# Kernel tuning notes

Measured on AMD Instinct MI355X. Metric: run time of the kernel, lower is better.

The kernel has to match this reference:

```python
import jax, jax.numpy as jnp
import numpy as np


def setup_inputs() -> dict:
    key = jax.random.key(0)
    B, S, H, O, L, NH = 16, 1024, 1024, 256, 4, 8
    ks = jax.random.split(key, 10)
    s = 0.02
    return {
        "x": jax.random.normal(ks[0], (B, S, H), dtype=jnp.float32),
        "Wf": jax.random.normal(ks[1], (L, H, H), dtype=jnp.float32) * s,
        "bf": jnp.zeros((L, H), dtype=jnp.float32),
        "Wi": jax.random.normal(ks[2], (L, H, H), dtype=jnp.float32) * s,
        "bi": jnp.zeros((L, H), dtype=jnp.float32),
        "Wh": jax.random.normal(ks[3], (L, H, H), dtype=jnp.float32) * s,
        "bh": jnp.zeros((L, H), dtype=jnp.float32),
        "in_proj_w": jax.random.normal(ks[4], (3 * H, H), dtype=jnp.float32) * s,
        "in_proj_b": jnp.zeros((3 * H,), dtype=jnp.float32),
        "out_w": jax.random.normal(ks[5], (H, H), dtype=jnp.float32) * s,
        "out_b": jnp.zeros((H,), dtype=jnp.float32),
        "fc_w": jax.random.normal(ks[6], (O, H), dtype=jnp.float32) * s,
        "fc_b": jnp.zeros((O,), dtype=jnp.float32),
    }


def _min_lstm_layer(x, Wf, bf, Wi, bi, Wh, bh):
    # x: [B, S, D] -> [B, S, H]. minLSTM: h_t = f'_t * h_{t-1} + i'_t * h~_t
    f = jax.nn.sigmoid(jnp.einsum("bsd,hd->bsh", x, Wf) + bf)
    i = jax.nn.sigmoid(jnp.einsum("bsd,hd->bsh", x, Wi) + bi)
    h_tilde = jnp.einsum("bsd,hd->bsh", x, Wh) + bh
    denom = f + i
    fp = f / denom                      # decay coefficient per step
    add = (i / denom) * h_tilde         # input contribution per step
    # sequential scan over time (linear gated recurrence)
    def step(h, inp):
        fp_t, add_t = inp               # each [B, H]
        h = fp_t * h + add_t
        return h, h
    B, S, H = fp.shape
    h0 = jnp.zeros((B, H), dtype=x.dtype)
    _, hs = jax.lax.scan(step, h0, (fp.transpose(1, 0, 2), add.transpose(1, 0, 2)))
    return hs.transpose(1, 0, 2)        # [B, S, H]


def _mhsa(x, in_proj_w, in_proj_b, out_w, out_b, num_heads=8):
    B, S, H = x.shape
    dh = H // num_heads
    qkv = jnp.einsum("bsh,oh->bso", x, in_proj_w) + in_proj_b  # [B,S,3H]
    q, k, v = jnp.split(qkv, 3, axis=-1)
    def heads(t):
        return t.reshape(B, S, num_heads, dh).transpose(0, 2, 1, 3)  # [B,nh,S,dh]
    q, k, v = heads(q), heads(k), heads(v)
    scores = jnp.einsum("bnqd,bnkd->bnqk", q, k) / jnp.sqrt(jnp.float32(dh)).astype(x.dtype)
    attn = jax.nn.softmax(scores, axis=-1)
    o = jnp.einsum("bnqk,bnkd->bnqd", attn, v)
    o = o.transpose(0, 2, 1, 3).reshape(B, S, H)
    return jnp.einsum("bsh,oh->bso", o, out_w) + out_b


def reference(x, Wf, bf, Wi, bi, Wh, bh, in_proj_w, in_proj_b, out_w, out_b, fc_w, fc_b):
    out = x
    L = Wf.shape[0]
    for l in range(L):
        out = _min_lstm_layer(out, Wf[l], bf[l], Wi[l], bi[l], Wh[l], bh[l])
    attn_out = _mhsa(out, in_proj_w, in_proj_b, out_w, out_b, num_heads=8)
    out = attn_out + out                 # dropout is identity at eval
    last = out[:, -1, :]                 # [B, H]
    return jnp.einsum("bh,oh->bo", last, fc_w) + fc_b
```

## Files before the change

kernel.cpp:

```cpp
#include <hip/hip_runtime.h>
#include <hip/hip_bf16.h>
#include <math.h>

#define Bq   16
#define Sq   1024
#define Hq   1024
#define Oq   256
#define Lq   4
#define NHq  8
#define DHq  128
#define Mq   (Bq*Sq)
#define HHq  (Hq*Hq)
#define NCc  32
#define CTc  32

typedef __bf16 bf16x8 __attribute__((ext_vector_type(8)));
typedef float  f32x4  __attribute__((ext_vector_type(4)));

__device__ __forceinline__ float bf2f(unsigned int u) {
    union { unsigned int i; float f; } x; x.i = u << 16; return x.f;
}
__device__ __forceinline__ unsigned short f2bf(float f) {
    union { float f; unsigned int i; } x; x.f = f;
    unsigned int r = x.i + 0x7fffu + ((x.i >> 16) & 1u);
    return (unsigned short)(r >> 16);
}
__device__ __forceinline__ float sigm(float x) { return 1.f / (1.f + __expf(-x)); }

__device__ __forceinline__ void gl2lds16(const unsigned short* g, unsigned short* l) {
    __builtin_amdgcn_global_load_lds((const __attribute__((address_space(1))) void*)g,
                                     (__attribute__((address_space(3))) void*)l, 16, 0, 0);
}

__global__ void cvt_kernel(const float* __restrict__ src, unsigned short* __restrict__ dst, int n) {
    int i = blockIdx.x * 256 + threadIdx.x;
    if (i < n) dst[i] = f2bf(src[i]);
}

__global__ void cvtW_kernel(const float* __restrict__ Wf, const float* __restrict__ Wi,
                            const float* __restrict__ Wh, unsigned short* __restrict__ Wcat) {
    int i = blockIdx.x * 256 + threadIdx.x;
    int l = (i >> 20) / 3;
    int r = i - l * 3 * HHq;
    int g = r >> 20; int j = r & (HHq - 1);
    const float* s = (g == 0) ? Wf : (g == 1) ? Wi : Wh;
    Wcat[i] = f2bf(s[(size_t)l * HHq + j]);
}

__global__ void bias3_kernel(const float* __restrict__ bf_, const float* __restrict__ bi_,
                             const float* __restrict__ bh_, float* __restrict__ out) {
    int i = blockIdx.x * 256 + threadIdx.x;
    int l = i / (3*Hq); int r = i % (3*Hq); int g = r >> 10; int j = r & (Hq-1);
    const float* s = (g == 0) ? bf_ : (g == 1) ? bi_ : bh_;
    out[i] = s[l*Hq + j];
}

__global__ __launch_bounds__(512, 1)
void gemm_gate_kernel(const unsigned short* __restrict__ A, const unsigned short* __restrict__ Wl,
                      const float* __restrict__ bias3, unsigned int* __restrict__ FA,
                      float* __restrict__ Ps, float* __restrict__ Asum)
{
    const int K = Hq;
    __shared__ unsigned short lds[4 * 20480];
    const int tid  = threadIdx.x;

    const int lid = blockIdx.x;
    const int xcd = lid & 7;
    const int s   = lid >> 3;
    const int bm  = xcd * 8 + (s >> 3);
    const int cb  = s & 7;

    const int wid  = tid >> 6, lane = tid & 63;
    const int wm   = (wid >> 2) * 128;
    const int wn   = (wid & 3) * 32;
    const int l15  = lane & 15, quad = lane >> 4;

    const unsigned short* Ag = A + (size_t)(bm*256) * K;

    const int lr   = lane >> 2;
    const int gc   = (lane & 3) ^ ((lane >> 3) & 3);
    int offA[2], ldsA[2];
    #pragma unroll
    for (int q = 0; q < 2; ++q) {
        int ra = wid*32 + q*16 + lr;
        offA[q] = ra * K + gc*8;
        ldsA[q] = (wid*32 + q*16) * 32;
    }
    int offW[3], ldsW[3];
    #pragma unroll
    for (int q = 0; q < 3; ++q) {
        int rw = wid*48 + q*16 + lr;
        int g  = rw >> 7;
        int nr = rw & 127;
        offW[q] = g * HHq + (cb*128 + nr) * K + gc*8;
        ldsW[q] = 8192 + (wid*48 + q*16) * 32;
    }

    const int crd = quad ^ ((l15 >> 1) & 3);

    f32x4 acc[3][8][2] = {};

    auto STAGE = [&](int kt, int slot) {
        const int kof = kt << 5;
        unsigned short* Sb = &lds[slot * 20480];
        #pragma unroll
        for (int q = 0; q < 2; ++q) gl2lds16(Ag + offA[q] + kof, Sb + ldsA[q]);
        #pragma unroll
        for (int q = 0; q < 3; ++q) gl2lds16(Wl + offW[q] + kof, Sb + ldsW[q]);
    };

    auto COMPUTE = [&](int slot) {
        const unsigned short* Sa = &lds[slot * 20480];
        const unsigned short* Sw = Sa + 8192;
        bf16x8 af[8];
        #pragma unroll
        for (int t = 0; t < 8; ++t)
            af[t] = *(const bf16x8*)&Sa[(wm + t*16 + l15)*32 + crd*8];
        __builtin_amdgcn_s_setprio(1);
        #pragma unroll
        for (int g = 0; g < 3; ++g) {
            bf16x8 wf[2];
            #pragma unroll
            for (int t = 0; t < 2; ++t)
                wf[t] = *(const bf16x8*)&Sw[(g*128 + wn + t*16 + l15)*32 + crd*8];
            #pragma unroll
            for (int tm = 0; tm < 8; ++tm)
                #pragma unroll
                for (int tn = 0; tn < 2; ++tn)
                    acc[g][tm][tn] = __builtin_amdgcn_mfma_f32_16x16x32_bf16(af[tm], wf[tn], acc[g][tm][tn], 0, 0, 0);
        }
        __builtin_amdgcn_s_setprio(0);
    };

    const int niter = K >> 5;

    STAGE(0, 0);
    STAGE(1, 1);

    for (int t = 0; t < niter - 2; ++t) {
        STAGE(t + 2, (t + 2) & 3);
        asm volatile("s_waitcnt vmcnt(10) lgkmcnt(0)" ::: "memory");
        __builtin_amdgcn_s_barrier();
        asm volatile("" ::: "memory");
        COMPUTE(t & 3);
    }
    asm volatile("s_waitcnt vmcnt(5) lgkmcnt(0)" ::: "memory");
    __builtin_amdgcn_s_barrier();
    asm volatile("" ::: "memory");
    COMPUTE((niter - 2) & 3);
    asm volatile("s_waitcnt vmcnt(0) lgkmcnt(0)" ::: "memory");
    __builtin_amdgcn_s_barrier();
    asm volatile("" ::: "memory");
    COMPUTE((niter - 1) & 3);

    const int colc0 = cb*128 + wn + l15;
    const int colc1 = colc0 + 16;
    float bf0 = bias3[colc0],      bf1 = bias3[colc1];
    float bi0 = bias3[Hq+colc0],   bi1 = bias3[Hq+colc1];
    float bh0 = bias3[2*Hq+colc0], bh1 = bias3[2*Hq+colc1];

    const int b_ = bm >> 2;
    const int chunkBase = (bm & 3) * 8 + (wm >> 5);

    #pragma unroll
    for (int cc = 0; cc < 4; ++cc) {
        float sP[2][2] = {{1.f,1.f},{1.f,1.f}};
        float sA[2][2] = {{0.f,0.f},{0.f,0.f}};
        #pragma unroll
        for (int sg = 0; sg < 2; ++sg) {
            int tm   = cc*2 + sg;
            int row0 = bm*256 + wm + tm*16 + quad*4;
            #pragma unroll
            for (int r = 0; r < 4; ++r) {
                #pragma unroll
                for (int tn = 0; tn < 2; ++tn) {
                    float bfv_ = tn ? bf1 : bf0;
                    float biv_ = tn ? bi1 : bi0;
                    float bhv_ = tn ? bh1 : bh0;
                    int   col  = tn ? colc1 : colc0;
                    float f  = sigm(acc[0][tm][tn][r] + bfv_);
                    float i  = sigm(acc[1][tm][tn][r] + biv_);
                    float ht = acc[2][tm][tn][r] + bhv_;
                    float rd = 1.f / (f + i);
                    unsigned short ufp = f2bf(f * rd);
                    unsigned short uad = f2bf(i * rd * ht);
                    FA[(size_t)(row0 + r) * Hq + col] =
                        (unsigned int)ufp | ((unsigned int)uad << 16);
                    float fpq = bf2f((unsigned int)ufp);
                    float adq = bf2f((unsigned int)uad);
                    sA[tn][sg] = fpq * sA[tn][sg] + adq;
                    sP[tn][sg] *= fpq;
                }
            }
        }
        int chunk  = chunkBase + cc;
        int oibase = (b_*NCc + chunk) * Hq;
        #pragma unroll
        for (int tn = 0; tn < 2; ++tn) {
            float P0 = sP[tn][0], A0 = sA[tn][0];
            float P1 = sP[tn][1], A1 = sA[tn][1];
            float pp, aa;
            pp = __shfl_up(P0, 16); aa = __shfl_up(A0, 16);
            if (quad >= 1) { A0 = P0*aa + A0; P0 = P0*pp; }
            pp = __shfl_up(P0, 32); aa = __shfl_up(A0, 32);
            if (quad >= 2) { A0 = P0*aa + A0; P0 = P0*pp; }
            pp = __shfl_up(P1, 16); aa = __shfl_up(A1, 16);
            if (quad >= 1) { A1 = P1*aa + A1; P1 = P1*pp; }
            pp = __shfl_up(P1, 32); aa = __shfl_up(A1, 32);
            if (quad >= 2) { A1 = P1*aa + A1; P1 = P1*pp; }
            float P0t = __shfl(P0, 48 + l15); float A0t = __shfl(A0, 48 + l15);
            float P1t = __shfl(P1, 48 + l15); float A1t = __shfl(A1, 48 + l15);
            if (quad == 0) {
                int col = tn ? colc1 : colc0;
                Ps[oibase + col]   = P1t * P0t;
                Asum[oibase + col] = P1t * A0t + A1t;
            }
        }
    }
}

__global__ __launch_bounds__(256, 2)
void gemm_bt_kernel(const unsigned short* __restrict__ A, const unsigned short* __restrict__ W,
                    const float* __restrict__ bias, unsigned short* __restrict__ C,
                    int N, int K, int nbn)
{
    __shared__ unsigned short lds[4 * 8192];
    const int tid  = threadIdx.x;

    const int lid = blockIdx.x;
    const int xcd = lid & 7;
    const int s   = lid >> 3;
    const int bm  = xcd * 16 + s / nbn;
    const int bn  = s % nbn;

    const int wid  = tid >> 6, lane = tid & 63;
    const int wm   = (wid >> 1) * 64, wn = (wid & 1) * 64;
    const int l15  = lane & 15, quad = lane >> 4;

    const unsigned short* Ag = A + (size_t)(bm*128) * K;
    const unsigned short* Wg = W + (size_t)(bn*128) * K;

    const int r0   = wid*32 + (lane >> 2);
    const int cst  = (lane & 3) ^ ((r0 >> 1) & 3);
    const int g0   = r0 * K + cst*8;
    const int g1   = (r0 + 16) * K + cst*8;
    const int lofs0 = wid*1024;
    const int lofs1 = wid*1024 + 512;

    const int crd = quad ^ ((l15 >> 1) & 3);

    f32x4 acc[4][4] = {};

    auto STAGE = [&](int kt, int slot) {
        const int kof = kt << 5;
        unsigned short* Sb = &lds[slot * 8192];
        gl2lds16(Ag + g0 + kof, Sb + lofs0);
        gl2lds16(Ag + g1 + kof, Sb + lofs1);
        gl2lds16(Wg + g0 + kof, Sb + 4096 + lofs0);
        gl2lds16(Wg + g1 + kof, Sb + 4096 + lofs1);
    };

    auto COMPUTE = [&](int slot) {
        const unsigned short* Sa = &lds[slot * 8192];
        const unsigned short* Sw = Sa + 4096;
        bf16x8 af[4], wf[4];
        #pragma unroll
        for (int t = 0; t < 4; ++t) {
            af[t] = *(const bf16x8*)&Sa[(wm + t*16 + l15)*32 + crd*8];
            wf[t] = *(const bf16x8*)&Sw[(wn + t*16 + l15)*32 + crd*8];
        }
        __builtin_amdgcn_s_setprio(1);
        #pragma unroll
        for (int tm = 0; tm < 4; ++tm)
            #pragma unroll
            for (int tn = 0; tn < 4; ++tn)
                acc[tm][tn] = __builtin_amdgcn_mfma_f32_16x16x32_bf16(af[tm], wf[tn], acc[tm][tn], 0, 0, 0);
        __builtin_amdgcn_s_setprio(0);
    };

    const int niter = K >> 5;

    STAGE(0, 0);
    STAGE(1, 1);

    for (int it = 0; it < niter - 2; ++it) {
        STAGE(it + 2, (it + 2) & 3);
        asm volatile("s_waitcnt vmcnt(8) lgkmcnt(0)" ::: "memory");
        __builtin_amdgcn_s_barrier();
        asm volatile("" ::: "memory");
        COMPUTE(it & 3);
    }
    asm volatile("s_waitcnt vmcnt(4) lgkmcnt(0)" ::: "memory");
    __builtin_amdgcn_s_barrier();
    asm volatile("" ::: "memory");
    COMPUTE((niter - 2) & 3);
    asm volatile("s_waitcnt vmcnt(0) lgkmcnt(0)" ::: "memory");
    __builtin_amdgcn_s_barrier();
    asm volatile("" ::: "memory");
    COMPUTE((niter - 1) & 3);

    #pragma unroll
    for (int tm = 0; tm < 4; ++tm) {
        int row0 = bm*128 + wm + tm*16 + quad*4;
        #pragma unroll
        for (int tn = 0; tn < 4; ++tn) {
            int col = bn*128 + wn + tn*16 + l15;
            float bv = bias[col];
            #pragma unroll
            for (int r = 0; r < 4; ++r)
                C[(size_t)(row0 + r) * N + col] = f2bf(acc[tm][tn][r] + bv);
        }
    }
}

__global__ void scan_base_kernel(const float* __restrict__ Ps, const float* __restrict__ Asum,
                                 float* __restrict__ Hb) {
    int t = blockIdx.x * 256 + threadIdx.x;
    int b = t >> 10, j = t & 1023;
    float h = 0.f;
    for (int c = 0; c < NCc; ++c) {
        int idx = (b*NCc + c)*Hq + j;
        Hb[idx] = h;
        h = Ps[idx] * h + Asum[idx];
    }
}

__global__ __launch_bounds__(256)
void scan_out_kernel(const unsigned int* __restrict__ FA,
                     const float* __restrict__ Hb, unsigned short* __restrict__ Ho) {
    int bid = blockIdx.x;
    int tid = threadIdx.x;
    int b = bid >> 6; int r = bid & 63; int chunk = r >> 1; int jb = r & 1;
    int j = jb*512 + tid*2;
    size_t base = ((size_t)(b*Sq + chunk*CTc)) * Hq + j;
    int oi = (b*NCc + chunk)*Hq + j;
    float h0 = Hb[oi], h1 = Hb[oi+1];
    for (int s = 0; s < CTc; ++s) {
        size_t ro = base + (size_t)s * Hq;
        uint2 v = *(const uint2*)(FA + ro);
        h0 = bf2f(v.x & 0xffffu) * h0 + bf2f(v.x >> 16);
        h1 = bf2f(v.y & 0xffffu) * h1 + bf2f(v.y >> 16);
        unsigned int packed = (unsigned int)f2bf(h0) | ((unsigned int)f2bf(h1) << 16);
        *(unsigned int*)(Ho + ro) = packed;
    }
}

__global__ void xlast_kernel(const unsigned short* __restrict__ act, float* __restrict__ xl) {
    int i = blockIdx.x * 256 + threadIdx.x;
    int b = i >> 10, j = i & 1023;
    xl[i] = bf2f((unsigned int)act[((size_t)(b*Sq + Sq-1)) * Hq + j]);
}

__global__ __launch_bounds__(256)
void gemv_kernel(const float* __restrict__ W, const float* __restrict__ xv,
                 const float* __restrict__ bias, const float* __restrict__ resid,
                 float* __restrict__ out, int N) {
    int b = blockIdx.x;
    int w = threadIdx.x >> 6, lane = threadIdx.x & 63;
    int n = blockIdx.y*4 + w;
    __shared__ float xs[Hq];
    *(float4*)&xs[threadIdx.x*4] = *(const float4*)&xv[(size_t)b*Hq + threadIdx.x*4];
    __syncthreads();
    const float4* wr = (const float4*)(W + (size_t)n * Hq);
    float a = 0.f;
    #pragma unroll
    for (int c = 0; c < 4; ++c) {
        float4 wv = wr[c*64 + lane];
        float4 x4 = *(const float4*)&xs[c*256 + lane*4];
        a += wv.x*x4.x + wv.y*x4.y + wv.z*x4.z + wv.w*x4.w;
    }
    #pragma unroll
    for (int st = 32; st > 0; st >>= 1) a += __shfl_xor(a, st, 64);
    if (lane == 0) out[(size_t)b*N + n] = a + bias[n] + (resid ? resid[(size_t)b*Hq + n] : 0.f);
}

__global__ __launch_bounds__(1024)
void attn_kernel(const unsigned short* __restrict__ KV,
                 const float* __restrict__ q, float* __restrict__ o) {
    int b = blockIdx.x >> 3, nh = blockIdx.x & 7;
    int tid = threadIdx.x;
    __shared__ float qs[DHq];
    __shared__ float p[Sq];
    __shared__ float redw[16];
    __shared__ float red2[16*DHq];
    if (tid < DHq) qs[tid] = q[b*Hq + nh*DHq + tid] * 0.08838834764831845f;
    __syncthreads();

    const int g = tid >> 4, l = tid & 15;
    const unsigned short* Kb = KV + (size_t)b*Sq*2048 + nh*DHq;
    float lmax = -1e30f;
    #pragma unroll 4
    for (int it = 0; it < 16; ++it) {
        int s = it*64 + g;
        union { uint4 v; unsigned short u[8]; } kk;
        kk.v = *(const uint4*)(Kb + (size_t)s*2048 + l*8);
        float a = 0.f;
        #pragma unroll
        for (int j = 0; j < 8; ++j) a += bf2f((unsigned int)kk.u[j]) * qs[l*8 + j];
        a += __shfl_xor(a, 1, 16);
        a += __shfl_xor(a, 2, 16);
        a += __shfl_xor(a, 4, 16);
        a += __shfl_xor(a, 8, 16);
        if (l == 0) p[s] = a;
        lmax = fmaxf(lmax, a);
    }
    #pragma unroll
    for (int st = 32; st > 0; st >>= 1) lmax = fmaxf(lmax, __shfl_xor(lmax, st, 64));
    if ((tid & 63) == 0) redw[tid >> 6] = lmax;
    __syncthreads();
    float mx = redw[0];
    #pragma unroll
    for (int i = 1; i < 16; ++i) mx = fmaxf(mx, redw[i]);

    float e = __expf(p[tid] - mx);
    float ls = e;
    #pragma unroll
    for (int st = 32; st > 0; st >>= 1) ls += __shfl_xor(ls, st, 64);
    __syncthreads();
    p[tid] = e;
    if ((tid & 63) == 0) redw[tid >> 6] = ls;
    __syncthreads();
    float ssum = 0.f;
    #pragma unroll
    for (int i = 0; i < 16; ++i) ssum += redw[i];
    float inv = 1.f / ssum;

    int d2 = (tid & 63) * 2, sb = tid >> 6;
    const unsigned short* Vb = KV + (size_t)b*Sq*2048 + 1024 + nh*DHq + d2;
    float a0 = 0.f, a1 = 0.f;
    for (int s = sb*64; s < sb*64 + 64; ++s) {
        unsigned int vv = *(const unsigned int*)(Vb + (size_t)s*2048);
        float pw = p[s];
        a0 += pw * bf2f(vv & 0xffffu);
        a1 += pw * bf2f(vv >> 16);
    }
    red2[sb*DHq + d2] = a0;
    red2[sb*DHq + d2 + 1] = a1;
    __syncthreads();
    if (tid < DHq) {
        float a = 0.f;
        #pragma unroll
        for (int i = 0; i < 16; ++i) a += red2[i*DHq + tid];
        o[b*Hq + nh*DHq + tid] = a * inv;
    }
}

extern "C" void kernel_launch(void* const* d_in, const int* in_sizes, int n_in,
                              void* d_out, int out_size, void* d_ws, size_t ws_size,
                              hipStream_t stream) {
    const float* x        = (const float*)d_in[0];
    const float* Wf       = (const float*)d_in[1];
    const float* bfv      = (const float*)d_in[2];
    const float* Wi       = (const float*)d_in[3];
    const float* biv      = (const float*)d_in[4];
    const float* Wh       = (const float*)d_in[5];
    const float* bhv      = (const float*)d_in[6];
    const float* in_proj_w= (const float*)d_in[7];
    const float* in_proj_b= (const float*)d_in[8];
    const float* out_w    = (const float*)d_in[9];
    const float* out_b    = (const float*)d_in[10];
    const float* fc_w     = (const float*)d_in[11];
    const float* fc_b     = (const float*)d_in[12];
    float* outp = (float*)d_out;

    char* p = (char*)d_ws;
    auto alloc = [&](size_t bytes) -> void* {
        void* r = (void*)p; p += (bytes + 255) & ~(size_t)255; return r;
    };
    unsigned short* Wcat = (unsigned short*)alloc((size_t)Lq*3*HHq*2);
    unsigned short* Wkv  = (unsigned short*)alloc((size_t)2048*Hq*2);
    float*          Bias3= (float*)alloc((size_t)Lq*3*Hq*4);
    unsigned short* actA = (unsigned short*)alloc((size_t)Mq*Hq*2);
    unsigned short* actB = (unsigned short*)alloc((size_t)Mq*Hq*2);
    unsigned int*   FAg  = (unsigned int*)alloc((size_t)Mq*Hq*4);
    float* Ps   = (float*)alloc((size_t)Bq*NCc*Hq*4);
    float* Asum = (float*)alloc((size_t)Bq*NCc*Hq*4);
    float* Hb   = (float*)alloc((size_t)Bq*NCc*Hq*4);
    unsigned short* KV = (unsigned short*)FAg;
    float* xl   = (float*)alloc((size_t)Bq*Hq*4);
    float* qbuf = (float*)alloc((size_t)Bq*Hq*4);
    float* obuf = (float*)alloc((size_t)Bq*Hq*4);
    float* rbuf = (float*)alloc((size_t)Bq*Hq*4);

    cvt_kernel<<<Mq*Hq/256, 256, 0, stream>>>(x, actA, Mq*Hq);
    cvtW_kernel<<<Lq*3*HHq/256, 256, 0, stream>>>(Wf, Wi, Wh, Wcat);
    cvt_kernel<<<2048*Hq/256, 256, 0, stream>>>(in_proj_w + (size_t)Hq*Hq, Wkv, 2048*Hq);
    bias3_kernel<<<(Lq*3*Hq)/256, 256, 0, stream>>>(bfv, biv, bhv, Bias3);

    unsigned short* cur = actA;
    unsigned short* nxt = actB;
    for (int l = 0; l < Lq; ++l) {
        gemm_gate_kernel<<<(Mq/256)*(Hq/128), 512, 0, stream>>>(
            cur, Wcat + (size_t)l*3*HHq, Bias3 + l*3*Hq, FAg, Ps, Asum);
        scan_base_kernel<<<Bq*Hq/256, 256, 0, stream>>>(Ps, Asum, Hb);
        scan_out_kernel<<<Bq*NCc*2, 256, 0, stream>>>(FAg, Hb, nxt);
        unsigned short* t = cur; cur = nxt; nxt = t;
    }

    gemm_bt_kernel<<<(Mq/128)*(2048/128), 256, 0, stream>>>(
        cur, Wkv, in_proj_b + Hq, KV, 2048, Hq, 2048/128);
    xlast_kernel<<<Bq*Hq/256, 256, 0, stream>>>(cur, xl);
    gemv_kernel<<<dim3(Bq, Hq/4), 256, 0, stream>>>(in_proj_w, xl, in_proj_b, nullptr, qbuf, Hq);
    attn_kernel<<<Bq*NHq, 1024, 0, stream>>>(KV, qbuf, obuf);
    gemv_kernel<<<dim3(Bq, Hq/4), 256, 0, stream>>>(out_w, obuf, out_b, xl, rbuf, Hq);
    gemv_kernel<<<dim3(Bq, Oq/4), 256, 0, stream>>>(fc_w, rbuf, fc_b, nullptr, outp, Oq);
}
```

Baseline: 815.4 us.

## Enlarge KV GEMM tile to 256x256 and fold scan base into scan output

The KV projection GEMM moves from 128x128 tiles with 4 waves to 256x256 tiles with 8 waves per block, doubling LDS staging and per-wave accumulators to raise operand reuse. The separate scan_base kernel is removed. Each scan_out block now recomputes its carry-in by serially combining the preceding chunk summaries, which saves one launch and the Hb round-trip but adds redundant work in later chunks. The larger GEMM tile raises register and LDS pressure and reduces occupancy to one block per CU.

Result: no change. 831.2 us (+1.9%).

```diff
diff --git a/kernel.cpp b/kernel.cpp
--- a/kernel.cpp
+++ b/kernel.cpp
@@ -219,59 +219,71 @@
     }
 }
 
-__global__ __launch_bounds__(256, 2)
+__global__ __launch_bounds__(512, 1)
 void gemm_bt_kernel(const unsigned short* __restrict__ A, const unsigned short* __restrict__ W,
                     const float* __restrict__ bias, unsigned short* __restrict__ C,
                     int N, int K, int nbn)
 {
-    __shared__ unsigned short lds[4 * 8192];
+    __shared__ unsigned short lds[4 * 16384];
     const int tid  = threadIdx.x;
 
     const int lid = blockIdx.x;
     const int xcd = lid & 7;
     const int s   = lid >> 3;
-    const int bm  = xcd * 16 + s / nbn;
+    const int bm  = xcd * 8 + s / nbn;
     const int bn  = s % nbn;
 
     const int wid  = tid >> 6, lane = tid & 63;
-    const int wm   = (wid >> 1) * 64, wn = (wid & 1) * 64;
+    const int wm   = (wid >> 2) * 128;
+    const int wn   = (wid & 3) * 64;
     const int l15  = lane & 15, quad = lane >> 4;
 
-    const unsigned short* Ag = A + (size_t)(bm*128) * K;
-    const unsigned short* Wg = W + (size_t)(bn*128) * K;
-
-    const int r0   = wid*32 + (lane >> 2);
-    const int cst  = (lane & 3) ^ ((r0 >> 1) & 3);
-    const int g0   = r0 * K + cst*8;
-    const int g1   = (r0 + 16) * K + cst*8;
-    const int lofs0 = wid*1024;
-    const int lofs1 = wid*1024 + 512;
+    const unsigned short* Ag = A + (size_t)(bm*256) * K;
+    const unsigned short* Wg = W + (size_t)(bn*256) * K;
+
+    const int lr   = lane >> 2;
+    const int gc   = (lane & 3) ^ ((lane >> 3) & 3);
+    int offA[2], ldsA[2];
+    #pragma unroll
+    for (int q = 0; q < 2; ++q) {
+        int ra = wid*32 + q*16 + lr;
+        offA[q] = ra * K + gc*8;
+        ldsA[q] = (wid*32 + q*16) * 32;
+    }
+    int offW[2], ldsW[2];
+    #pragma unroll
+    for (int q = 0; q < 2; ++q) {
+        int rw = wid*32 + q*16 + lr;
+        offW[q] = rw * K + gc*8;
+        ldsW[q] = 8192 + (wid*32 + q*16) * 32;
+    }
 
     const int crd = quad ^ ((l15 >> 1) & 3);
 
-    f32x4 acc[4][4] = {};
+    f32x4 acc[8][4] = {};
 
     auto STAGE = [&](int kt, int slot) {
         const int kof = kt << 5;
-        unsigned short* Sb = &lds[slot * 8192];
-        gl2lds16(Ag + g0 + kof, Sb + lofs0);
-        gl2lds16(Ag + g1 + kof, Sb + lofs1);
-        gl2lds16(Wg + g0 + kof, Sb + 4096 + lofs0);
-        gl2lds16(Wg + g1 + kof, Sb + 4096 + lofs1);
+        unsigned short* Sb = &lds[slot * 16384];
+        #pragma unroll
+        for (int q = 0; q < 2; ++q) gl2lds16(Ag + offA[q] + kof, Sb + ldsA[q]);
+        #pragma unroll
+        for (int q = 0; q < 2; ++q) gl2lds16(Wg + offW[q] + kof, Sb + ldsW[q]);
     };
 
     auto COMPUTE = [&](int slot) {
-        const unsigned short* Sa = &lds[slot * 8192];
-        const unsigned short* Sw = Sa + 4096;
-        bf16x8 af[4], wf[4];
-        #pragma unroll
-        for (int t = 0; t < 4; ++t) {
+        const unsigned short* Sa = &lds[slot * 16384];
+        const unsigned short* Sw = Sa + 8192;
+        bf16x8 af[8], wf[4];
+        #pragma unroll
+        for (int t = 0; t < 8; ++t)
             af[t] = *(const bf16x8*)&Sa[(wm + t*16 + l15)*32 + crd*8];
+        #pragma unroll
+        for (int t = 0; t < 4; ++t)
             wf[t] = *(const bf16x8*)&Sw[(wn + t*16 + l15)*32 + crd*8];
-        }
         __builtin_amdgcn_s_setprio(1);
         #pragma unroll
-        for (int tm = 0; tm < 4; ++tm)
+        for (int tm = 0; tm < 8; ++tm)
             #pragma unroll
             for (int tn = 0; tn < 4; ++tn)
                 acc[tm][tn] = __builtin_amdgcn_mfma_f32_16x16x32_bf16(af[tm], wf[tn], acc[tm][tn], 0, 0, 0);
@@ -300,11 +312,11 @@
     COMPUTE((niter - 1) & 3);
 
     #pragma unroll
-    for (int tm = 0; tm < 4; ++tm) {
-        int row0 = bm*128 + wm + tm*16 + quad*4;
+    for (int tm = 0; tm < 8; ++tm) {
+        int row0 = bm*256 + wm + tm*16 + quad*4;
         #pragma unroll
         for (int tn = 0; tn < 4; ++tn) {
-            int col = bn*128 + wn + tn*16 + l15;
+            int col = bn*256 + wn + tn*16 + l15;
             float bv = bias[col];
             #pragma unroll
             for (int r = 0; r < 4; ++r)
@@ -313,28 +325,25 @@
     }
 }
 
-__global__ void scan_base_kernel(const float* __restrict__ Ps, const float* __restrict__ Asum,
-                                 float* __restrict__ Hb) {
-    int t = blockIdx.x * 256 + threadIdx.x;
-    int b = t >> 10, j = t & 1023;
-    float h = 0.f;
-    for (int c = 0; c < NCc; ++c) {
-        int idx = (b*NCc + c)*Hq + j;
-        Hb[idx] = h;
-        h = Ps[idx] * h + Asum[idx];
-    }
-}
-
 __global__ __launch_bounds__(256)
 void scan_out_kernel(const unsigned int* __restrict__ FA,
-                     const float* __restrict__ Hb, unsigned short* __restrict__ Ho) {
+                     const float* __restrict__ Ps, const float* __restrict__ Asum,
+                     unsigned short* __restrict__ Ho) {
     int bid = blockIdx.x;
     int tid = threadIdx.x;
     int b = bid >> 6; int r = bid & 63; int chunk = r >> 1; int jb = r & 1;
     int j = jb*512 + tid*2;
     size_t base = ((size_t)(b*Sq + chunk*CTc)) * Hq + j;
-    int oi = (b*NCc + chunk)*Hq + j;
-    float h0 = Hb[oi], h1 = Hb[oi+1];
+
+    float h0 = 0.f, h1 = 0.f;
+    for (int c = 0; c < chunk; ++c) {
+        int idx = (b*NCc + c)*Hq + j;
+        float2 P = *(const float2*)&Ps[idx];
+        float2 Aa = *(const float2*)&Asum[idx];
+        h0 = P.x * h0 + Aa.x;
+        h1 = P.y * h1 + Aa.y;
+    }
+
     for (int s = 0; s < CTc; ++s) {
         size_t ro = base + (size_t)s * Hq;
         uint2 v = *(const uint2*)(FA + ro);
@@ -475,7 +484,6 @@
     unsigned int*   FAg  = (unsigned int*)alloc((size_t)Mq*Hq*4);
     float* Ps   = (float*)alloc((size_t)Bq*NCc*Hq*4);
     float* Asum = (float*)alloc((size_t)Bq*NCc*Hq*4);
-    float* Hb   = (float*)alloc((size_t)Bq*NCc*Hq*4);
     unsigned short* KV = (unsigned short*)FAg;
     float* xl   = (float*)alloc((size_t)Bq*Hq*4);
     float* qbuf = (float*)alloc((size_t)Bq*Hq*4);
@@ -492,13 +500,12 @@
     for (int l = 0; l < Lq; ++l) {
         gemm_gate_kernel<<<(Mq/256)*(Hq/128), 512, 0, stream>>>(
             cur, Wcat + (size_t)l*3*HHq, Bias3 + l*3*Hq, FAg, Ps, Asum);
-        scan_base_kernel<<<Bq*Hq/256, 256, 0, stream>>>(Ps, Asum, Hb);
-        scan_out_kernel<<<Bq*NCc*2, 256, 0, stream>>>(FAg, Hb, nxt);
+        scan_out_kernel<<<Bq*NCc*2, 256, 0, stream>>>(FAg, Ps, Asum, nxt);
         unsigned short* t = cur; cur = nxt; nxt = t;
     }
 
-    gemm_bt_kernel<<<(Mq/128)*(2048/128), 256, 0, stream>>>(
-        cur, Wkv, in_proj_b + Hq, KV, 2048, Hq, 2048/128);
+    gemm_bt_kernel<<<(Mq/256)*(2048/256), 512, 0, stream>>>(
+        cur, Wkv, in_proj_b + Hq, KV, 2048, Hq, 2048/256);
     xlast_kernel<<<Bq*Hq/256, 256, 0, stream>>>(cur, xl);
     gemv_kernel<<<dim3(Bq, Hq/4), 256, 0, stream>>>(in_proj_w, xl, in_proj_b, nullptr, qbuf, Hq);
     attn_kernel<<<Bq*NHq, 1024, 0, stream>>>(KV, qbuf, obuf);
```
